# Optimization experiments

Measured on AMD Instinct MI355X. Metric: run time of the kernel, lower is better.

## Reference

```python
import jax, jax.numpy as jnp
import numpy as np

N_NODES = 100000
N_EDGES = 1600000
IN_DIM = 256
HID = 64
HEADS = 2
OUT_DIM = 256
NEG_SLOPE = 0.2  # DGL GATConv default


def setup_inputs() -> dict:
    key = jax.random.key(0)
    ks = jax.random.split(key, 10)
    feat = jax.random.normal(ks[0], (N_NODES, IN_DIM), dtype=jnp.float32)
    src = jax.random.randint(ks[1], (N_EDGES,), 0, N_NODES)
    dst = jax.random.randint(ks[2], (N_EDGES,), 0, N_NODES)
    W = jax.random.normal(ks[3], (IN_DIM, HEADS * HID), dtype=jnp.float32) * 0.05
    attn_l = jax.random.normal(ks[4], (HEADS, HID), dtype=jnp.float32) * 0.05
    attn_r = jax.random.normal(ks[5], (HEADS, HID), dtype=jnp.float32) * 0.05
    gat_bias = jnp.zeros((HEADS * HID,), dtype=jnp.float32)
    lin_W = jax.random.normal(ks[6], (HEADS * HID, OUT_DIM), dtype=jnp.float32) * 0.05
    lin_b = jnp.zeros((OUT_DIM,), dtype=jnp.float32)
    return {"feat": feat, "src": src, "dst": dst, "W": W, "attn_l": attn_l,
            "attn_r": attn_r, "gat_bias": gat_bias, "lin_W": lin_W, "lin_b": lin_b}


def reference(feat, src, dst, W, attn_l, attn_r, gat_bias, lin_W, lin_b):
    N = feat.shape[0]
    H, D = attn_l.shape
    # GATConv: linear projection -> [N, H, D]
    h = (feat @ W).reshape(N, H, D)
    el = jnp.sum(h * attn_l[None], axis=-1)  # [N, H]
    er = jnp.sum(h * attn_r[None], axis=-1)  # [N, H]
    # per-edge attention logits, LeakyReLU
    e = jax.nn.leaky_relu(el[src] + er[dst], NEG_SLOPE)  # [E, H]
    # edge softmax over incoming edges of each dst node
    m = jax.ops.segment_max(e, dst, num_segments=N)      # [N, H] (-inf for isolated nodes, unused)
    ee = jnp.exp(e - m[dst])
    s = jax.ops.segment_sum(ee, dst, num_segments=N)
    alpha = ee / s[dst]                                   # [E, H]
    # weighted aggregation: scatter-add messages to dst
    out = jax.ops.segment_sum(alpha[:, :, None] * h[src], dst, num_segments=N)  # [N, H, D]
    out = out + gat_bias.reshape(1, H, D)
    out = jax.nn.relu(out.reshape(N, H * D))
    return jax.nn.relu(out @ lin_W + lin_b)
```

## Files before the change

kernel.cpp:

```cpp
#include <hip/hip_runtime.h>

#define N_NODES 100000
#define N_EDGES 1600000
#define IN_DIM 256
#define HID 64
#define HEADS 2
#define HD 128
#define OUT_DIM 256
#define NEG_SLOPE 0.2f

typedef unsigned int uint32;
typedef unsigned short ushort16;
typedef __attribute__((ext_vector_type(8))) short bf16x8;
typedef __attribute__((ext_vector_type(4))) float f32x4;

__device__ __forceinline__ ushort16 f2bf(float f) {
    union { float f; uint32 u; } v; v.f = f;
    uint32 u = v.u;
    return (ushort16)((u + 0x7FFFu + ((u >> 16) & 1u)) >> 16);
}
__device__ __forceinline__ float bf2f(ushort16 b) {
    union { uint32 u; float f; } v; v.u = ((uint32)b) << 16;
    return v.f;
}

__global__ __launch_bounds__(256)
void conv_w1(const float* __restrict__ W, ushort16* __restrict__ Wt)
{
    int idx = blockIdx.x * 256 + threadIdx.x;
    int n = idx >> 8, k = idx & 255;
    Wt[idx] = f2bf(W[k * HD + n]);
}
__global__ __launch_bounds__(256)
void conv_w2(const float* __restrict__ W, ushort16* __restrict__ Wt)
{
    int idx = blockIdx.x * 256 + threadIdx.x;
    int n = idx >> 7, k = idx & 127;
    Wt[idx] = f2bf(W[k * OUT_DIM + n]);
}

__global__ __launch_bounds__(256)
void gemm1_mfma(const float* __restrict__ A, const ushort16* __restrict__ Bt,
                ushort16* __restrict__ C, int M)
{
    __shared__ char alds[2 * 16384];
    const int t    = threadIdx.x;
    const int lane = t & 63;
    const int w    = t >> 6;
    const int wr   = w >> 1, wc = w & 1;
    const int m0   = blockIdx.x * 128;
    const int l15  = lane & 15;
    const int lq   = lane >> 4;

    f32x4 acc[4][4] = {};
    float4 av[8];

#define G1_LOAD(KT)                                                               \
    {                                                                             \
        _Pragma("unroll")                                                         \
        for (int i = 0; i < 8; i++) {                                             \
            int flat = t + i * 256;                                               \
            int r = flat >> 4, kq = (flat & 15) * 4;                              \
            int gr = m0 + r; if (gr >= M) gr = M - 1;                             \
            av[i] = *reinterpret_cast<const float4*>(                             \
                        &A[(size_t)gr * IN_DIM + (KT) * 64 + kq]);                \
        }                                                                         \
    }
#define G1_WRITE(BUF)                                                             \
    {                                                                             \
        _Pragma("unroll")                                                         \
        for (int i = 0; i < 8; i++) {                                             \
            int flat = t + i * 256;                                               \
            int r = flat >> 4, kq = (flat & 15) * 4;                              \
            uint2 p;                                                              \
            p.x = (uint32)f2bf(av[i].x) | ((uint32)f2bf(av[i].y) << 16);          \
            p.y = (uint32)f2bf(av[i].z) | ((uint32)f2bf(av[i].w) << 16);          \
            int byte = (r * 128 + kq * 2) ^ ((r & 7) << 4);                       \
            *reinterpret_cast<uint2*>(&alds[(BUF) * 16384 + byte]) = p;           \
        }                                                                         \
    }

    G1_LOAD(0); G1_WRITE(0);
    __syncthreads();
    int cur = 0;
    for (int kt = 0; kt < 4; kt++) {
        if (kt < 3) G1_LOAD(kt + 1);
        bf16x8 bfr[2][4];
#pragma unroll
        for (int ks = 0; ks < 2; ks++)
#pragma unroll
            for (int nf = 0; nf < 4; nf++) {
                int col = wc * 64 + nf * 16 + l15;
                int kb  = (kt * 2 + ks) * 32 + lq * 8;
                bfr[ks][nf] = *reinterpret_cast<const bf16x8*>(&Bt[(size_t)col * 256 + kb]);
            }
#pragma unroll
        for (int ks = 0; ks < 2; ks++) {
            bf16x8 afr[4];
#pragma unroll
            for (int mf = 0; mf < 4; mf++) {
                int row  = wr * 64 + mf * 16 + l15;
                int byte = (row * 128 + ks * 64 + lq * 16) ^ ((row & 7) << 4);
                afr[mf] = *reinterpret_cast<const bf16x8*>(&alds[cur * 16384 + byte]);
            }
#pragma unroll
            for (int mf = 0; mf < 4; mf++)
#pragma unroll
                for (int nf = 0; nf < 4; nf++)
                    acc[mf][nf] = __builtin_amdgcn_mfma_f32_16x16x32_bf16(
                        afr[mf], bfr[ks][nf], acc[mf][nf], 0, 0, 0);
        }
        if (kt < 3) G1_WRITE(cur ^ 1);
        __syncthreads();
        cur ^= 1;
    }
#pragma unroll
    for (int mf = 0; mf < 4; mf++)
#pragma unroll
        for (int nf = 0; nf < 4; nf++)
#pragma unroll
            for (int q = 0; q < 4; q++) {
                int row = m0 + wr * 64 + mf * 16 + lq * 4 + q;
                int col = wc * 64 + nf * 16 + l15;
                if (row < M) C[(size_t)row * HD + col] = f2bf(acc[mf][nf][q]);
            }
#undef G1_LOAD
#undef G1_WRITE
}

__global__ __launch_bounds__(256)
void gemm2_mfma(const ushort16* __restrict__ Ahi, const ushort16* __restrict__ Alo,
                const ushort16* __restrict__ Bt, const float* __restrict__ bias,
                float* __restrict__ Cout, int M)
{
    __shared__ char alds[2 * 32768];
    const int t    = threadIdx.x;
    const int lane = t & 63;
    const int w    = t >> 6;
    const int wr   = w >> 1, wc = w & 1;
    const int m0   = blockIdx.x * 128;
    const int n0   = blockIdx.y * 128;
    const int l15  = lane & 15;
    const int lq   = lane >> 4;

    f32x4 acc[4][4] = {};

#pragma unroll
    for (int p = 0; p < 2; p++) {
        const ushort16* src = p ? Alo : Ahi;
#pragma unroll
        for (int i = 0; i < 8; i++) {
            int flat = t + i * 256;
            int r = flat >> 4, e8 = (flat & 15) * 8;
            int gr = m0 + r; if (gr >= M) gr = M - 1;
            uint4 v = *reinterpret_cast<const uint4*>(&src[(size_t)gr * HD + e8]);
            int byte = (r * 256 + e8 * 2) ^ ((r & 7) << 4);
            *reinterpret_cast<uint4*>(&alds[p * 32768 + byte]) = v;
        }
    }
    bf16x8 bfr[4][4];
#pragma unroll
    for (int ks = 0; ks < 4; ks++)
#pragma unroll
        for (int nf = 0; nf < 4; nf++) {
            int col = n0 + wc * 64 + nf * 16 + l15;
            int kb  = ks * 32 + lq * 8;
            bfr[ks][nf] = *reinterpret_cast<const bf16x8*>(&Bt[(size_t)col * HD + kb]);
        }
    __syncthreads();

#pragma unroll
    for (int pass = 0; pass < 2; pass++) {
#pragma unroll
        for (int ks = 0; ks < 4; ks++) {
            bf16x8 afr[4];
#pragma unroll
            for (int mf = 0; mf < 4; mf++) {
                int row  = wr * 64 + mf * 16 + l15;
                int byte = (row * 256 + ks * 64 + lq * 16) ^ ((row & 7) << 4);
                afr[mf] = *reinterpret_cast<const bf16x8*>(&alds[pass * 32768 + byte]);
            }
#pragma unroll
            for (int mf = 0; mf < 4; mf++)
#pragma unroll
                for (int nf = 0; nf < 4; nf++)
                    acc[mf][nf] = __builtin_amdgcn_mfma_f32_16x16x32_bf16(
                        afr[mf], bfr[ks][nf], acc[mf][nf], 0, 0, 0);
        }
    }

    float bias_v[4];
#pragma unroll
    for (int nf = 0; nf < 4; nf++) bias_v[nf] = bias[n0 + wc * 64 + nf * 16 + l15];
#pragma unroll
    for (int mf = 0; mf < 4; mf++)
#pragma unroll
        for (int nf = 0; nf < 4; nf++)
#pragma unroll
            for (int q = 0; q < 4; q++) {
                int row = m0 + wr * 64 + mf * 16 + lq * 4 + q;
                int col = n0 + wc * 64 + nf * 16 + l15;
                if (row < M)
                    Cout[(size_t)row * OUT_DIM + col] = fmaxf(acc[mf][nf][q] + bias_v[nf], 0.f);
            }
}

__global__ __launch_bounds__(256)
void elr_kernel(const ushort16* __restrict__ hb, const float* __restrict__ attn_l,
                const float* __restrict__ attn_r, float* __restrict__ el,
                float* __restrict__ er)
{
    int w    = (int)((blockIdx.x * blockDim.x + threadIdx.x) >> 6);
    int lane = threadIdx.x & 63;
    if (w >= N_NODES) return;
    float h0 = bf2f(hb[(size_t)w * HD + lane]);
    float h1 = bf2f(hb[(size_t)w * HD + 64 + lane]);
    float v0 = h0 * attn_l[lane];
    float v1 = h1 * attn_l[64 + lane];
    float v2 = h0 * attn_r[lane];
    float v3 = h1 * attn_r[64 + lane];
#pragma unroll
    for (int o = 32; o; o >>= 1) {
        v0 += __shfl_xor(v0, o);
        v1 += __shfl_xor(v1, o);
        v2 += __shfl_xor(v2, o);
        v3 += __shfl_xor(v3, o);
    }
    if (lane == 0) {
        el[w * 2 + 0] = v0; el[w * 2 + 1] = v1;
        er[w * 2 + 0] = v2; er[w * 2 + 1] = v3;
    }
}

__global__ void deg_kernel(const int* __restrict__ dst, int* __restrict__ deg)
{
    int i = blockIdx.x * blockDim.x + threadIdx.x;
    if (i < N_EDGES) atomicAdd(&deg[dst[i]], 1);
}

#define SCAN_B 1024
#define SCAN_NB ((N_NODES + SCAN_B - 1) / SCAN_B)

__global__ __launch_bounds__(SCAN_B)
void scan_part(const int* __restrict__ deg, int* __restrict__ row_ptr,
               int* __restrict__ bsum)
{
    __shared__ int sdata[SCAN_B];
    const int t = threadIdx.x, b = blockIdx.x;
    const int i = b * SCAN_B + t;
    int v = (i < N_NODES) ? deg[i] : 0;
    sdata[t] = v;
    __syncthreads();
    for (int off = 1; off < SCAN_B; off <<= 1) {
        int x = 0;
        if (t >= off) x = sdata[t - off];
        __syncthreads();
        sdata[t] += x;
        __syncthreads();
    }
    if (i < N_NODES) row_ptr[i] = sdata[t] - v;
    if (t == SCAN_B - 1) bsum[b] = sdata[t];
}

__global__ __launch_bounds__(128)
void scan_top(int* __restrict__ bsum, int* __restrict__ row_ptr)
{
    __shared__ int sdata[128];
    const int t = threadIdx.x;
    int v = (t < SCAN_NB) ? bsum[t] : 0;
    sdata[t] = v;
    __syncthreads();
    for (int off = 1; off < 128; off <<= 1) {
        int x = 0;
        if (t >= off) x = sdata[t - off];
        __syncthreads();
        sdata[t] += x;
        __syncthreads();
    }
    if (t < SCAN_NB) bsum[t] = sdata[t] - v;
    if (t == 127) row_ptr[N_NODES] = sdata[127];
}

__global__ __launch_bounds__(SCAN_B)
void scan_add(int* __restrict__ row_ptr, const int* __restrict__ bsum)
{
    const int i = blockIdx.x * SCAN_B + threadIdx.x;
    if (i < N_NODES) row_ptr[i] += bsum[blockIdx.x];
}

__global__ void scatter_kernel(const int* __restrict__ src, const int* __restrict__ dst,
                               const int* __restrict__ row_ptr, int* __restrict__ cursor,
                               int* __restrict__ sorted_src)
{
    int i = blockIdx.x * blockDim.x + threadIdx.x;
    if (i < N_EDGES) {
        int d = dst[i];
        int p = row_ptr[d] + atomicAdd(&cursor[d], 1);
        sorted_src[p] = src[i];
    }
}

__global__ __launch_bounds__(256)
void node_kernel(const ushort16* __restrict__ hb, const float* __restrict__ el,
                 const float* __restrict__ er, const int* __restrict__ row_ptr,
                 const int* __restrict__ sorted_src, float* __restrict__ ws_e,
                 const float* __restrict__ gat_bias,
                 ushort16* __restrict__ agg_hi, ushort16* __restrict__ agg_lo)
{
    int n    = (int)((blockIdx.x * blockDim.x + threadIdx.x) >> 6);
    int lane = threadIdx.x & 63;
    if (n >= N_NODES) return;
    int beg = row_ptr[n], end = row_ptr[n + 1];

    float er0 = er[n * 2 + 0], er1 = er[n * 2 + 1];

    float mx0 = -1e30f, mx1 = -1e30f, s0 = 0.f, s1 = 0.f;
    for (int i = beg + lane; i < end; i += 64) {
        int s = sorted_src[i];
        float2 elv = *reinterpret_cast<const float2*>(&el[s * 2]);
        float e0 = elv.x + er0; e0 = e0 > 0.f ? e0 : NEG_SLOPE * e0;
        float e1 = elv.y + er1; e1 = e1 > 0.f ? e1 : NEG_SLOPE * e1;
        float2 st; st.x = e0; st.y = e1;
        *reinterpret_cast<float2*>(&ws_e[(size_t)i * 2]) = st;
        float m0n = fmaxf(mx0, e0);
        s0 = s0 * __expf(mx0 - m0n) + __expf(e0 - m0n);
        mx0 = m0n;
        float m1n = fmaxf(mx1, e1);
        s1 = s1 * __expf(mx1 - m1n) + __expf(e1 - m1n);
        mx1 = m1n;
    }
#pragma unroll
    for (int o = 32; o; o >>= 1) {
        float mo0 = __shfl_xor(mx0, o);
        float so0 = __shfl_xor(s0, o);
        float m0  = fmaxf(mx0, mo0);
        s0 = s0 * __expf(mx0 - m0) + so0 * __expf(mo0 - m0);
        mx0 = m0;
        float mo1 = __shfl_xor(mx1, o);
        float so1 = __shfl_xor(s1, o);
        float m1  = fmaxf(mx1, mo1);
        s1 = s1 * __expf(mx1 - m1) + so1 * __expf(mo1 - m1);
        mx1 = m1;
    }
    __threadfence_block();

    float inv0 = s0 > 0.f ? 1.f / s0 : 0.f;
    float inv1 = s1 > 0.f ? 1.f / s1 : 0.f;

    const int half = lane >> 5;
    const int j    = lane & 31;
    const bool hd1 = (j >= 16);
    const float mxh  = hd1 ? mx1 : mx0;
    const float invh = hd1 ? inv1 : inv0;
    float4 acc = {0.f, 0.f, 0.f, 0.f};

    int e = beg + half;
#define EDGE_BODY(E)                                                              \
    {                                                                             \
        float2 ev = *reinterpret_cast<const float2*>(&ws_e[(size_t)(E) * 2]);     \
        int s = sorted_src[(E)];                                                  \
        float a = __expf((hd1 ? ev.y : ev.x) - mxh) * invh;                       \
        uint2 hv = *reinterpret_cast<const uint2*>(&hb[(size_t)s * HD + 4 * j]);  \
        acc.x = fmaf(a, bf2f((ushort16)(hv.x & 0xffff)), acc.x);                  \
        acc.y = fmaf(a, bf2f((ushort16)(hv.x >> 16)),    acc.y);                  \
        acc.z = fmaf(a, bf2f((ushort16)(hv.y & 0xffff)), acc.z);                  \
        acc.w = fmaf(a, bf2f((ushort16)(hv.y >> 16)),    acc.w);                  \
    }
    for (; e + 2 < end; e += 4) { EDGE_BODY(e); EDGE_BODY(e + 2); }
    if (e < end) EDGE_BODY(e);
#undef EDGE_BODY

    acc.x += __shfl_xor(acc.x, 32);
    acc.y += __shfl_xor(acc.y, 32);
    acc.z += __shfl_xor(acc.z, 32);
    acc.w += __shfl_xor(acc.w, 32);

    if (lane < 32) {
        float4 b = *reinterpret_cast<const float4*>(&gat_bias[4 * j]);
        float o[4];
        o[0] = fmaxf(acc.x + b.x, 0.f);
        o[1] = fmaxf(acc.y + b.y, 0.f);
        o[2] = fmaxf(acc.z + b.z, 0.f);
        o[3] = fmaxf(acc.w + b.w, 0.f);
        ushort16 hi[4], lo[4];
#pragma unroll
        for (int q = 0; q < 4; q++) {
            hi[q] = f2bf(o[q]);
            lo[q] = f2bf(o[q] - bf2f(hi[q]));
        }
        uint2 ph, pl;
        ph.x = (uint32)hi[0] | ((uint32)hi[1] << 16);
        ph.y = (uint32)hi[2] | ((uint32)hi[3] << 16);
        pl.x = (uint32)lo[0] | ((uint32)lo[1] << 16);
        pl.y = (uint32)lo[2] | ((uint32)lo[3] << 16);
        *reinterpret_cast<uint2*>(&agg_hi[(size_t)n * HD + 4 * j]) = ph;
        *reinterpret_cast<uint2*>(&agg_lo[(size_t)n * HD + 4 * j]) = pl;
    }
}

extern "C" void kernel_launch(void* const* d_in, const int* in_sizes, int n_in,
                              void* d_out, int out_size, void* d_ws, size_t ws_size,
                              hipStream_t stream)
{
    const float* feat     = (const float*)d_in[0];
    const int*   src      = (const int*)d_in[1];
    const int*   dst      = (const int*)d_in[2];
    const float* W        = (const float*)d_in[3];
    const float* attn_l   = (const float*)d_in[4];
    const float* attn_r   = (const float*)d_in[5];
    const float* gat_bias = (const float*)d_in[6];
    const float* lin_W    = (const float*)d_in[7];
    const float* lin_b    = (const float*)d_in[8];
    float* out = (float*)d_out;

    char* ws = (char*)d_ws;
    ushort16* hb     = (ushort16*)(ws + 0);
    ushort16* agg_hi = (ushort16*)(ws + 25600000);
    ushort16* agg_lo = (ushort16*)(ws + 51200000);
    float* ws_e   = (float*)(ws + 76800000);
    int*   ssrc   = (int*)  (ws + 89600000);
    float* el     = (float*)(ws + 96000000);
    float* er     = (float*)(ws + 96800000);
    int*   deg    = (int*)  (ws + 97600000);
    int*   cursor = (int*)  (ws + 98000000);
    int*   rowptr = (int*)  (ws + 98400000);
    int*   bsum   = (int*)  (ws + 98800128);
    ushort16* Wt1 = (ushort16*)(ws + 98804608);
    ushort16* Wt2 = (ushort16*)(ws + 98870144);

    hipMemsetAsync(deg, 0, 800000, stream);

    conv_w1<<<128, 256, 0, stream>>>(W, Wt1);
    conv_w2<<<128, 256, 0, stream>>>(lin_W, Wt2);

    dim3 blk(256);
    gemm1_mfma<<<(N_NODES + 127) / 128, blk, 0, stream>>>(feat, Wt1, hb, N_NODES);

    elr_kernel<<<(N_NODES + 3) / 4, 256, 0, stream>>>(hb, attn_l, attn_r, el, er);

    deg_kernel<<<(N_EDGES + 255) / 256, 256, 0, stream>>>(dst, deg);
    scan_part<<<SCAN_NB, SCAN_B, 0, stream>>>(deg, rowptr, bsum);
    scan_top<<<1, 128, 0, stream>>>(bsum, rowptr);
    scan_add<<<SCAN_NB, SCAN_B, 0, stream>>>(rowptr, bsum);
    scatter_kernel<<<(N_EDGES + 255) / 256, 256, 0, stream>>>(src, dst, rowptr, cursor, ssrc);

    node_kernel<<<(N_NODES + 3) / 4, 256, 0, stream>>>(hb, el, er, rowptr, ssrc, ws_e,
                                                       gat_bias, agg_hi, agg_lo);

    dim3 g2((N_NODES + 127) / 128, 2);
    gemm2_mfma<<<g2, blk, 0, stream>>>(agg_hi, agg_lo, Wt2, lin_b, out, N_NODES);
}
```

Before: 380.0 us.

## Precompute normalized edge weights and widen aggregation to 16-byte gathers

The aggregation kernel first computes the normalized attention coefficients once per edge and writes them back into the edge workspace. The gather loop then reads those finished weights instead of recomputing an exp per lane per edge. Each lane now loads 8 bf16 values (uint4) per neighbor row, so 4 edges are processed concurrently per wavefront rather than 2. The cost is an extra pass that reads and writes the edge weights, plus a two-step shuffle reduction.

```diff
diff --git a/kernel.cpp b/kernel.cpp
--- a/kernel.cpp
+++ b/kernel.cpp
@@ -21,6 +21,14 @@
 }
 __device__ __forceinline__ float bf2f(ushort16 b) {
     union { uint32 u; float f; } v; v.u = ((uint32)b) << 16;
+    return v.f;
+}
+__device__ __forceinline__ float bflo(uint32 u) {
+    union { uint32 u; float f; } v; v.u = u << 16;
+    return v.f;
+}
+__device__ __forceinline__ float bfhi(uint32 u) {
+    union { uint32 u; float f; } v; v.u = u & 0xffff0000u;
     return v.f;
 }
 
@@ -342,59 +350,78 @@
         s1 = s1 * __expf(mx1 - m1) + so1 * __expf(mo1 - m1);
         mx1 = m1;
     }
-    __threadfence_block();
 
     float inv0 = s0 > 0.f ? 1.f / s0 : 0.f;
     float inv1 = s1 > 0.f ? 1.f / s1 : 0.f;
 
-    const int half = lane >> 5;
-    const int j    = lane & 31;
-    const bool hd1 = (j >= 16);
-    const float mxh  = hd1 ? mx1 : mx0;
-    const float invh = hd1 ? inv1 : inv0;
-    float4 acc = {0.f, 0.f, 0.f, 0.f};
-
-    int e = beg + half;
+    for (int i = beg + lane; i < end; i += 64) {
+        float2 ev = *reinterpret_cast<const float2*>(&ws_e[(size_t)i * 2]);
+        float2 av;
+        av.x = __expf(ev.x - mx0) * inv0;
+        av.y = __expf(ev.y - mx1) * inv1;
+        *reinterpret_cast<float2*>(&ws_e[(size_t)i * 2]) = av;
+    }
+    __threadfence_block();
+
+    const int slot = lane >> 4;
+    const int j    = lane & 15;
+    float acc[8] = {0.f, 0.f, 0.f, 0.f, 0.f, 0.f, 0.f, 0.f};
+
 #define EDGE_BODY(E)                                                              \
     {                                                                             \
-        float2 ev = *reinterpret_cast<const float2*>(&ws_e[(size_t)(E) * 2]);     \
+        float2 av = *reinterpret_cast<const float2*>(&ws_e[(size_t)(E) * 2]);     \
         int s = sorted_src[(E)];                                                  \
-        float a = __expf((hd1 ? ev.y : ev.x) - mxh) * invh;                       \
-        uint2 hv = *reinterpret_cast<const uint2*>(&hb[(size_t)s * HD + 4 * j]);  \
-        acc.x = fmaf(a, bf2f((ushort16)(hv.x & 0xffff)), acc.x);                  \
-        acc.y = fmaf(a, bf2f((ushort16)(hv.x >> 16)),    acc.y);                  \
-        acc.z = fmaf(a, bf2f((ushort16)(hv.y & 0xffff)), acc.z);                  \
-        acc.w = fmaf(a, bf2f((ushort16)(hv.y >> 16)),    acc.w);                  \
-    }
-    for (; e + 2 < end; e += 4) { EDGE_BODY(e); EDGE_BODY(e + 2); }
+        float a = (j < 8) ? av.x : av.y;                                          \
+        uint4 hv = *reinterpret_cast<const uint4*>(&hb[(size_t)s * HD + 8 * j]);  \
+        acc[0] = fmaf(a, bflo(hv.x), acc[0]);                                     \
+        acc[1] = fmaf(a, bfhi(hv.x), acc[1]);                                     \
+        acc[2] = fmaf(a, bflo(hv.y), acc[2]);                                     \
+        acc[3] = fmaf(a, bfhi(hv.y), acc[3]);                                     \
+        acc[4] = fmaf(a, bflo(hv.z), acc[4]);                                     \
+        acc[5] = fmaf(a, bfhi(hv.z), acc[5]);                                     \
+        acc[6] = fmaf(a, bflo(hv.w), acc[6]);                                     \
+        acc[7] = fmaf(a, bfhi(hv.w), acc[7]);                                     \
+    }
+    int e = beg + slot;
+    for (; e + 4 < end; e += 8) { EDGE_BODY(e); EDGE_BODY(e + 4); }
     if (e < end) EDGE_BODY(e);
 #undef EDGE_BODY
 
-    acc.x += __shfl_xor(acc.x, 32);
-    acc.y += __shfl_xor(acc.y, 32);
-    acc.z += __shfl_xor(acc.z, 32);
-    acc.w += __shfl_xor(acc.w, 32);
-
-    if (lane < 32) {
-        float4 b = *reinterpret_cast<const float4*>(&gat_bias[4 * j]);
-        float o[4];
-        o[0] = fmaxf(acc.x + b.x, 0.f);
-        o[1] = fmaxf(acc.y + b.y, 0.f);
-        o[2] = fmaxf(acc.z + b.z, 0.f);
-        o[3] = fmaxf(acc.w + b.w, 0.f);
-        ushort16 hi[4], lo[4];
-#pragma unroll
-        for (int q = 0; q < 4; q++) {
+#pragma unroll
+    for (int q = 0; q < 8; q++) {
+        acc[q] += __shfl_xor(acc[q], 16);
+        acc[q] += __shfl_xor(acc[q], 32);
+    }
+
+    if (lane < 16) {
+        float4 b0 = *reinterpret_cast<const float4*>(&gat_bias[8 * j]);
+        float4 b1 = *reinterpret_cast<const float4*>(&gat_bias[8 * j + 4]);
+        float o[8];
+        o[0] = fmaxf(acc[0] + b0.x, 0.f);
+        o[1] = fmaxf(acc[1] + b0.y, 0.f);
+        o[2] = fmaxf(acc[2] + b0.z, 0.f);
+        o[3] = fmaxf(acc[3] + b0.w, 0.f);
+        o[4] = fmaxf(acc[4] + b1.x, 0.f);
+        o[5] = fmaxf(acc[5] + b1.y, 0.f);
+        o[6] = fmaxf(acc[6] + b1.z, 0.f);
+        o[7] = fmaxf(acc[7] + b1.w, 0.f);
+        uint4 ph, pl;
+        ushort16 hi[8], lo[8];
+#pragma unroll
+        for (int q = 0; q < 8; q++) {
             hi[q] = f2bf(o[q]);
             lo[q] = f2bf(o[q] - bf2f(hi[q]));
         }
-        uint2 ph, pl;
         ph.x = (uint32)hi[0] | ((uint32)hi[1] << 16);
         ph.y = (uint32)hi[2] | ((uint32)hi[3] << 16);
+        ph.z = (uint32)hi[4] | ((uint32)hi[5] << 16);
+        ph.w = (uint32)hi[6] | ((uint32)hi[7] << 16);
         pl.x = (uint32)lo[0] | ((uint32)lo[1] << 16);
         pl.y = (uint32)lo[2] | ((uint32)lo[3] << 16);
-        *reinterpret_cast<uint2*>(&agg_hi[(size_t)n * HD + 4 * j]) = ph;
-        *reinterpret_cast<uint2*>(&agg_lo[(size_t)n * HD + 4 * j]) = pl;
+        pl.z = (uint32)lo[4] | ((uint32)lo[5] << 16);
+        pl.w = (uint32)lo[6] | ((uint32)lo[7] << 16);
+        *reinterpret_cast<uint4*>(&agg_hi[(size_t)n * HD + 8 * j]) = ph;
+        *reinterpret_cast<uint4*>(&agg_lo[(size_t)n * HD + 8 * j]) = pl;
     }
 }
 
```

Result: faster. 370.2 us (-2.6%).
